# Optimization experiments

Measured on AMD Instinct MI355X. Metric: run time of the kernel, lower is better.

Reference implementation:

```python
import jax, jax.numpy as jnp
import numpy as np

N = 50000
E = 800000
EPS = 1e-16
NEG_SLOPE = 0.2

def setup_inputs() -> dict:
    key = jax.random.key(0)
    ks = jax.random.split(key, 10)
    s = lambda fan: 1.0 / np.sqrt(fan)
    return {
        "x": jax.random.normal(ks[0], (N, 128), dtype=jnp.float32),
        "edge_index": jax.random.randint(ks[1], (2, E), 0, N, dtype=jnp.int64),
        "W1": jax.random.normal(ks[2], (128, 4 * 32), dtype=jnp.float32) * s(128),
        "att_src1": jax.random.normal(ks[3], (4, 32), dtype=jnp.float32) * s(32),
        "att_dst1": jax.random.normal(ks[4], (4, 32), dtype=jnp.float32) * s(32),
        "b1": jnp.zeros((128,), dtype=jnp.float32),
        "W2": jax.random.normal(ks[5], (128, 2), dtype=jnp.float32) * s(128),
        "att_src2": jax.random.normal(ks[6], (1, 2), dtype=jnp.float32) * s(2),
        "att_dst2": jax.random.normal(ks[7], (1, 2), dtype=jnp.float32) * s(2),
        "b2": jnp.zeros((2,), dtype=jnp.float32),
    }

def _gat_conv(x, src, dst, W, att_src, att_dst, bias, heads, out_ch, concat):
    n = x.shape[0]
    h = (x @ W).reshape(n, heads, out_ch)                      # [N,H,C]
    a_src = jnp.sum(h * att_src[None], axis=-1)                # [N,H]
    a_dst = jnp.sum(h * att_dst[None], axis=-1)                # [N,H]
    e = jax.nn.leaky_relu(a_src[src] + a_dst[dst], NEG_SLOPE)  # [Etot,H]
    # segment softmax over incoming edges per destination node
    m = jax.ops.segment_max(e, dst, num_segments=n)            # [N,H]
    m = jnp.where(jnp.isfinite(m), m, 0.0)
    ex = jnp.exp(e - m[dst])
    denom = jax.ops.segment_sum(ex, dst, num_segments=n)       # [N,H]
    alpha = ex / (denom[dst] + EPS)                            # [Etot,H]
    out = jax.ops.segment_sum(alpha[:, :, None] * h[src], dst, num_segments=n)  # [N,H,C]
    if concat:
        out = out.reshape(n, heads * out_ch)
    else:
        out = out.mean(axis=1)
    return out + bias

def reference(x, edge_index, W1, att_src1, att_dst1, b1, W2, att_src2, att_dst2, b2):
    n = x.shape[0]
    # PyG GATConv adds self-loops by default
    loops = jnp.arange(n, dtype=edge_index.dtype)
    src = jnp.concatenate([edge_index[0], loops])
    dst = jnp.concatenate([edge_index[1], loops])
    # dropout is identity at inference
    h = jax.nn.elu(_gat_conv(x, src, dst, W1, att_src1, att_dst1, b1, 4, 32, True))
    h = _gat_conv(h, src, dst, W2, att_src2, att_dst2, b2, 1, 2, False)
    return jax.nn.log_softmax(h, axis=1)
```

## Files before the change

kernel.cpp:

```cpp
#include <hip/hip_runtime.h>
#include <hip/hip_bf16.h>

#define NN 50000
#define EE 800000
#define CAP 64
#define CSTRIDE 16
#define NEG_SLOPE 0.2f
#define EPSF 1e-16f
#define BUILD_BLOCKS 4096
#define GEMM_BLOCKS ((NN + 63) / 64)
#define NPAIRS (EE / 2)

typedef unsigned int uint32;
typedef __attribute__((ext_vector_type(8))) short short8;
typedef __attribute__((ext_vector_type(4))) float floatx4;

__device__ __forceinline__ unsigned short f2bf(float f) {
  unsigned int u = __float_as_uint(f);
  unsigned int r = (u + 0x7fffu + ((u >> 16) & 1u)) >> 16;
  return (unsigned short)r;
}
__device__ __forceinline__ float bf_lo(uint32 v) { return __uint_as_float(v << 16); }
__device__ __forceinline__ float bf_hi(uint32 v) { return __uint_as_float(v & 0xffff0000u); }
__device__ __forceinline__ float lrelu(float e) { return fmaxf(e, NEG_SLOPE * e); }

__global__ __launch_bounds__(256) void prep_zero_k(
    const float* __restrict__ W1, unsigned short* __restrict__ Wt,
    int* __restrict__ counts) {
  const int step = gridDim.x * 256;
  const int t0 = blockIdx.x * 256 + threadIdx.x;
  for (int i = t0; i < NN * CSTRIDE; i += step)
    counts[i] = ((i & (CSTRIDE - 1)) == 0) ? 1 : 0;
  for (int i = t0; i < 128 * 128; i += step) {
    int k = i >> 7, c = i & 127;
    Wt[c * 128 + k] = f2bf(W1[i]);
  }
}

__device__ __forceinline__ void do_build(int b, const int* __restrict__ ei,
                                         int* __restrict__ counts,
                                         int* __restrict__ csr) {
  const int range = b & 7;
  const int lo = range * (NN / 8);
  const int hi = lo + (NN / 8);
  const int group = b >> 3;
  const int tid0 = group * 256 + threadIdx.x;
  const int stride = (BUILD_BLOCKS >> 3) * 256;

  { int n = lo + tid0; if (n < hi) csr[n * CAP] = n; }

  const int2* __restrict__ dst2 = (const int2*)(ei + EE);
  const int2* __restrict__ src2 = (const int2*)(ei);
  for (int p = tid0; p < NPAIRS; p += stride) {
    int2 d2 = dst2[p];
    int2 s2 = src2[p];
    if (d2.x >= lo && d2.x < hi) {
      int r = atomicAdd(&counts[d2.x * CSTRIDE], 1);
      if (r < CAP) csr[d2.x * CAP + r] = s2.x;
    }
    if (d2.y >= lo && d2.y < hi) {
      int r = atomicAdd(&counts[d2.y * CSTRIDE], 1);
      if (r < CAP) csr[d2.y * CAP + r] = s2.y;
    }
  }
}

__device__ __forceinline__ void do_gemm_tile(
    int tile, const float* __restrict__ x, const unsigned short* __restrict__ Wt,
    const float* __restrict__ att_src1, const float* __restrict__ att_dst1,
    uint32* __restrict__ h1b, float* __restrict__ as1, float* __restrict__ ad1) {
  const int t    = threadIdx.x;
  const int wave = t >> 6;
  const int lane = t & 63;
  const int quad = lane >> 4;
  const int col  = lane & 15;
  const int nodeBase = tile * 64 + wave * 16;

  floatx4 acc[8];
  #pragma unroll
  for (int i = 0; i < 8; i++) acc[i] = (floatx4){0.f, 0.f, 0.f, 0.f};

  int mread = nodeBase + col; if (mread >= NN) mread = NN - 1;
  const float* __restrict__ xrow = x + (size_t)mread * 128 + quad * 8;
  const unsigned short* __restrict__ bbase = Wt + col * 128 + quad * 8;

  #pragma unroll
  for (int ks = 0; ks < 4; ks++) {
    float4 a0 = *(const float4*)(xrow + ks * 32);
    float4 a1 = *(const float4*)(xrow + ks * 32 + 4);
    union { short8 v; unsigned short u[8]; } af;
    af.u[0] = f2bf(a0.x); af.u[1] = f2bf(a0.y);
    af.u[2] = f2bf(a0.z); af.u[3] = f2bf(a0.w);
    af.u[4] = f2bf(a1.x); af.u[5] = f2bf(a1.y);
    af.u[6] = f2bf(a1.z); af.u[7] = f2bf(a1.w);
    #pragma unroll
    for (int tt = 0; tt < 8; tt++) {
      short8 bf = *(const short8*)(bbase + tt * 16 * 128 + ks * 32);
      acc[tt] = __builtin_amdgcn_mfma_f32_16x16x32_bf16(af.v, bf, acc[tt], 0, 0, 0);
    }
  }

  float asv[8], adv[8];
  #pragma unroll
  for (int tt = 0; tt < 8; tt++) {
    asv[tt] = att_src1[tt * 16 + col];
    adv[tt] = att_dst1[tt * 16 + col];
  }

  #pragma unroll
  for (int r = 0; r < 4; r++) {
    const int gn = nodeBase + quad * 4 + r;
    const bool live = (gn < NN);
    #pragma unroll
    for (int tt = 0; tt < 8; tt++) {
      float v = acc[tt][r];
      float w = __shfl_xor(v, 1, 64);
      if (live && ((col & 1) == 0)) {
        uint32 pk = (uint32)f2bf(v) | ((uint32)f2bf(w) << 16);
        h1b[(size_t)gn * 64 + tt * 8 + (col >> 1)] = pk;
      }
    }
    #pragma unroll
    for (int h = 0; h < 4; h++) {
      float ps = acc[2 * h][r] * asv[2 * h] + acc[2 * h + 1][r] * asv[2 * h + 1];
      float pd = acc[2 * h][r] * adv[2 * h] + acc[2 * h + 1][r] * adv[2 * h + 1];
      #pragma unroll
      for (int off = 1; off < 16; off <<= 1) {
        ps += __shfl_xor(ps, off, 64);
        pd += __shfl_xor(pd, off, 64);
      }
      if (live && col == 0) {
        as1[gn * 4 + h] = ps;
        ad1[gn * 4 + h] = pd;
      }
    }
  }
}

__global__ __launch_bounds__(256) void work_k(
    const int* __restrict__ ei, int* __restrict__ counts, int* __restrict__ csr,
    const float* __restrict__ x, const unsigned short* __restrict__ Wt,
    const float* __restrict__ att_src1, const float* __restrict__ att_dst1,
    uint32* __restrict__ h1b, float* __restrict__ as1, float* __restrict__ ad1) {
  const int b = blockIdx.x;
  if (b < BUILD_BLOCKS) {
    do_build(b, ei, counts, csr);
  } else {
    do_gemm_tile(b - BUILD_BLOCKS, x, Wt, att_src1, att_dst1, h1b, as1, ad1);
  }
}

__global__ __launch_bounds__(256) void agg1_k(
    const int* __restrict__ counts, const int* __restrict__ csr,
    const uint32* __restrict__ h1b, const float* __restrict__ as1,
    const float* __restrict__ ad1, const float* __restrict__ b1,
    const float* __restrict__ W2, const float* __restrict__ att_src2,
    const float* __restrict__ att_dst2, float4* __restrict__ rec) {
  const int lane = threadIdx.x & 63;
  const int wv = threadIdx.x >> 6;
  const int hd = lane >> 4;
  const int n = __builtin_amdgcn_readfirstlane(blockIdx.x * 4 + wv);

  int cnt = counts[n * CSTRIDE];
  cnt = __builtin_amdgcn_readfirstlane(cnt < CAP ? cnt : CAP);
  const int* __restrict__ row = csr + n * CAP;
  const float adv = ad1[n * 4 + hd];

  float den = 0.f, accx = 0.f, accy = 0.f;
  int j = 0;
  for (; j + 3 < cnt; j += 4) {
    int s0 = __builtin_amdgcn_readfirstlane(row[j]);
    int s1 = __builtin_amdgcn_readfirstlane(row[j + 1]);
    int s2 = __builtin_amdgcn_readfirstlane(row[j + 2]);
    int s3 = __builtin_amdgcn_readfirstlane(row[j + 3]);
    float e0 = as1[s0 * 4 + hd] + adv;
    float e1 = as1[s1 * 4 + hd] + adv;
    float e2 = as1[s2 * 4 + hd] + adv;
    float e3 = as1[s3 * 4 + hd] + adv;
    uint32 v0 = h1b[s0 * 64 + lane];
    uint32 v1 = h1b[s1 * 64 + lane];
    uint32 v2 = h1b[s2 * 64 + lane];
    uint32 v3 = h1b[s3 * 64 + lane];
    e0 = lrelu(e0); e1 = lrelu(e1); e2 = lrelu(e2); e3 = lrelu(e3);
    float x0 = __expf(e0), x1 = __expf(e1), x2 = __expf(e2), x3 = __expf(e3);
    den += (x0 + x1) + (x2 + x3);
    accx = fmaf(x0, bf_lo(v0), accx);
    accy = fmaf(x0, bf_hi(v0), accy);
    accx = fmaf(x1, bf_lo(v1), accx);
    accy = fmaf(x1, bf_hi(v1), accy);
    accx = fmaf(x2, bf_lo(v2), accx);
    accy = fmaf(x2, bf_hi(v2), accy);
    accx = fmaf(x3, bf_lo(v3), accx);
    accy = fmaf(x3, bf_hi(v3), accy);
  }
  for (; j < cnt; j++) {
    int s = __builtin_amdgcn_readfirstlane(row[j]);
    float e = lrelu(as1[s * 4 + hd] + adv);
    float ex = __expf(e);
    uint32 v = h1b[s * 64 + lane];
    den += ex;
    accx = fmaf(ex, bf_lo(v), accx);
    accy = fmaf(ex, bf_hi(v), accy);
  }

  float inv = 1.f / (den + EPSF);
  float2 bb = ((const float2*)b1)[lane];
  float ox = accx * inv + bb.x;
  float oy = accy * inv + bb.y;
  ox = (ox > 0.f) ? ox : (__expf(ox) - 1.f);
  oy = (oy > 0.f) ? oy : (__expf(oy) - 1.f);

  float4 wq = ((const float4*)W2)[lane];
  float p0 = ox * wq.x + oy * wq.z;
  float p1 = ox * wq.y + oy * wq.w;
  #pragma unroll
  for (int off = 32; off; off >>= 1) {
    p0 += __shfl_xor(p0, off, 64);
    p1 += __shfl_xor(p1, off, 64);
  }
  if (lane == 0) {
    rec[n] = make_float4(p0, p1,
                         p0 * att_src2[0] + p1 * att_src2[1],
                         p0 * att_dst2[0] + p1 * att_dst2[1]);
  }
}

__global__ __launch_bounds__(256) void agg2_k(
    const int* __restrict__ counts, const int* __restrict__ csr,
    const float4* __restrict__ rec, const float* __restrict__ b2,
    float* __restrict__ out) {
  int i = blockIdx.x * 256 + threadIdx.x;
  if (i >= NN * 8) return;
  int n = i >> 3;
  int sub = i & 7;
  const float adv = rec[n].w;
  int cnt = counts[n * CSTRIDE];
  cnt = cnt < CAP ? cnt : CAP;
  const int* __restrict__ row = csr + n * CAP;

  float den = 0.f, a0 = 0.f, a1 = 0.f;
  for (int j = sub; j < cnt; j += 8) {
    int s = row[j];
    float4 rs = rec[s];
    float e = lrelu(rs.z + adv);
    float ex = __expf(e);
    den += ex;
    a0 = fmaf(ex, rs.x, a0);
    a1 = fmaf(ex, rs.y, a1);
  }
  #pragma unroll
  for (int off = 4; off; off >>= 1) {
    den += __shfl_down(den, off, 8);
    a0  += __shfl_down(a0, off, 8);
    a1  += __shfl_down(a1, off, 8);
  }
  if (sub == 0) {
    float inv = 1.f / (den + EPSF);
    float o0 = a0 * inv + b2[0];
    float o1 = a1 * inv + b2[1];
    float mx = fmaxf(o0, o1);
    float lse = mx + __logf(__expf(o0 - mx) + __expf(o1 - mx));
    *(float2*)&out[n * 2] = make_float2(o0 - lse, o1 - lse);
  }
}

extern "C" void kernel_launch(void* const* d_in, const int* in_sizes, int n_in,
                              void* d_out, int out_size, void* d_ws, size_t ws_size,
                              hipStream_t stream) {
  const float* x        = (const float*)d_in[0];
  const int*   ei       = (const int*)d_in[1];
  const float* W1       = (const float*)d_in[2];
  const float* att_src1 = (const float*)d_in[3];
  const float* att_dst1 = (const float*)d_in[4];
  const float* b1       = (const float*)d_in[5];
  const float* W2       = (const float*)d_in[6];
  const float* att_src2 = (const float*)d_in[7];
  const float* att_dst2 = (const float*)d_in[8];
  const float* b2       = (const float*)d_in[9];
  float* out = (float*)d_out;

  char* p = (char*)d_ws;
  auto alloc = [&](size_t bytes) {
    char* r = p;
    p += (bytes + 255) & ~size_t(255);
    return r;
  };
  uint32* h1b  = (uint32*)alloc(sizeof(uint32) * NN * 64);
  float* as1   = (float*)alloc(sizeof(float) * NN * 4);
  float* ad1   = (float*)alloc(sizeof(float) * NN * 4);
  float4* rec  = (float4*)alloc(sizeof(float4) * NN);
  int*   counts = (int*)alloc(sizeof(int) * NN * CSTRIDE);
  int*   csr   = (int*)alloc(sizeof(int) * NN * CAP);
  unsigned short* Wt = (unsigned short*)alloc(sizeof(unsigned short) * 128 * 128);

  prep_zero_k<<<512, 256, 0, stream>>>(W1, Wt, counts);
  work_k<<<BUILD_BLOCKS + GEMM_BLOCKS, 256, 0, stream>>>(
      ei, counts, csr, x, Wt, att_src1, att_dst1, h1b, as1, ad1);
  agg1_k<<<NN / 4, 256, 0, stream>>>(counts, csr, h1b, as1, ad1, b1, W2,
                                     att_src2, att_dst2, rec);
  agg2_k<<<(NN * 8 + 255) / 256, 256, 0, stream>>>(counts, csr, rec, b2, out);
}
```

Before: 188.9 us.

## Fold W1 transpose into GEMM blocks via LDS and replace prep kernel with memset

Result: faster. 172.1 us (-8.9%).

```diff
diff --git a/kernel.cpp b/kernel.cpp
--- a/kernel.cpp
+++ b/kernel.cpp
@@ -10,6 +10,7 @@
 #define BUILD_BLOCKS 4096
 #define GEMM_BLOCKS ((NN + 63) / 64)
 #define NPAIRS (EE / 2)
+#define WROW 136
 
 typedef unsigned int uint32;
 typedef __attribute__((ext_vector_type(8))) short short8;
@@ -23,19 +24,6 @@
 __device__ __forceinline__ float bf_lo(uint32 v) { return __uint_as_float(v << 16); }
 __device__ __forceinline__ float bf_hi(uint32 v) { return __uint_as_float(v & 0xffff0000u); }
 __device__ __forceinline__ float lrelu(float e) { return fmaxf(e, NEG_SLOPE * e); }
-
-__global__ __launch_bounds__(256) void prep_zero_k(
-    const float* __restrict__ W1, unsigned short* __restrict__ Wt,
-    int* __restrict__ counts) {
-  const int step = gridDim.x * 256;
-  const int t0 = blockIdx.x * 256 + threadIdx.x;
-  for (int i = t0; i < NN * CSTRIDE; i += step)
-    counts[i] = ((i & (CSTRIDE - 1)) == 0) ? 1 : 0;
-  for (int i = t0; i < 128 * 128; i += step) {
-    int k = i >> 7, c = i & 127;
-    Wt[c * 128 + k] = f2bf(W1[i]);
-  }
-}
 
 __device__ __forceinline__ void do_build(int b, const int* __restrict__ ei,
                                          int* __restrict__ counts,
@@ -56,17 +44,17 @@
     int2 s2 = src2[p];
     if (d2.x >= lo && d2.x < hi) {
       int r = atomicAdd(&counts[d2.x * CSTRIDE], 1);
-      if (r < CAP) csr[d2.x * CAP + r] = s2.x;
+      if (r < CAP - 1) csr[d2.x * CAP + r + 1] = s2.x;
     }
     if (d2.y >= lo && d2.y < hi) {
       int r = atomicAdd(&counts[d2.y * CSTRIDE], 1);
-      if (r < CAP) csr[d2.y * CAP + r] = s2.y;
+      if (r < CAP - 1) csr[d2.y * CAP + r + 1] = s2.y;
     }
   }
 }
 
 __device__ __forceinline__ void do_gemm_tile(
-    int tile, const float* __restrict__ x, const unsigned short* __restrict__ Wt,
+    int tile, const float* __restrict__ x, const unsigned short* __restrict__ WtL,
     const float* __restrict__ att_src1, const float* __restrict__ att_dst1,
     uint32* __restrict__ h1b, float* __restrict__ as1, float* __restrict__ ad1) {
   const int t    = threadIdx.x;
@@ -82,7 +70,7 @@
 
   int mread = nodeBase + col; if (mread >= NN) mread = NN - 1;
   const float* __restrict__ xrow = x + (size_t)mread * 128 + quad * 8;
-  const unsigned short* __restrict__ bbase = Wt + col * 128 + quad * 8;
+  const unsigned short* __restrict__ bbase = WtL + col * WROW + quad * 8;
 
   #pragma unroll
   for (int ks = 0; ks < 4; ks++) {
@@ -95,7 +83,7 @@
     af.u[6] = f2bf(a1.z); af.u[7] = f2bf(a1.w);
     #pragma unroll
     for (int tt = 0; tt < 8; tt++) {
-      short8 bf = *(const short8*)(bbase + tt * 16 * 128 + ks * 32);
+      short8 bf = *(const short8*)(bbase + tt * 16 * WROW + ks * 32);
       acc[tt] = __builtin_amdgcn_mfma_f32_16x16x32_bf16(af.v, bf, acc[tt], 0, 0, 0);
     }
   }
@@ -139,14 +127,28 @@
 
 __global__ __launch_bounds__(256) void work_k(
     const int* __restrict__ ei, int* __restrict__ counts, int* __restrict__ csr,
-    const float* __restrict__ x, const unsigned short* __restrict__ Wt,
+    const float* __restrict__ x, const float* __restrict__ W1,
     const float* __restrict__ att_src1, const float* __restrict__ att_dst1,
     uint32* __restrict__ h1b, float* __restrict__ as1, float* __restrict__ ad1) {
+  __shared__ unsigned short WtL[128 * WROW];
   const int b = blockIdx.x;
-  if (b < BUILD_BLOCKS) {
-    do_build(b, ei, counts, csr);
+  if (b < GEMM_BLOCKS) {
+    const int c  = threadIdx.x & 127;
+    const int kh = (threadIdx.x >> 7) * 4;
+    #pragma unroll
+    for (int k0 = kh; k0 < 128; k0 += 8) {
+      unsigned short w0 = f2bf(W1[(k0 + 0) * 128 + c]);
+      unsigned short w1 = f2bf(W1[(k0 + 1) * 128 + c]);
+      unsigned short w2 = f2bf(W1[(k0 + 2) * 128 + c]);
+      unsigned short w3 = f2bf(W1[(k0 + 3) * 128 + c]);
+      uint32 lo = (uint32)w0 | ((uint32)w1 << 16);
+      uint32 hi = (uint32)w2 | ((uint32)w3 << 16);
+      *(uint2*)&WtL[c * WROW + k0] = make_uint2(lo, hi);
+    }
+    __syncthreads();
+    do_gemm_tile(b, x, WtL, att_src1, att_dst1, h1b, as1, ad1);
   } else {
-    do_gemm_tile(b - BUILD_BLOCKS, x, Wt, att_src1, att_dst1, h1b, as1, ad1);
+    do_build(b - GEMM_BLOCKS, ei, counts, csr);
   }
 }
 
@@ -161,7 +163,7 @@
   const int hd = lane >> 4;
   const int n = __builtin_amdgcn_readfirstlane(blockIdx.x * 4 + wv);
 
-  int cnt = counts[n * CSTRIDE];
+  int cnt = counts[n * CSTRIDE] + 1;
   cnt = __builtin_amdgcn_readfirstlane(cnt < CAP ? cnt : CAP);
   const int* __restrict__ row = csr + n * CAP;
   const float adv = ad1[n * 4 + hd];
@@ -234,7 +236,7 @@
   int n = i >> 3;
   int sub = i & 7;
   const float adv = rec[n].w;
-  int cnt = counts[n * CSTRIDE];
+  int cnt = counts[n * CSTRIDE] + 1;
   cnt = cnt < CAP ? cnt : CAP;
   const int* __restrict__ row = csr + n * CAP;
 
@@ -291,11 +293,10 @@
   float4* rec  = (float4*)alloc(sizeof(float4) * NN);
   int*   counts = (int*)alloc(sizeof(int) * NN * CSTRIDE);
   int*   csr   = (int*)alloc(sizeof(int) * NN * CAP);
-  unsigned short* Wt = (unsigned short*)alloc(sizeof(unsigned short) * 128 * 128);
-
-  prep_zero_k<<<512, 256, 0, stream>>>(W1, Wt, counts);
-  work_k<<<BUILD_BLOCKS + GEMM_BLOCKS, 256, 0, stream>>>(
-      ei, counts, csr, x, Wt, att_src1, att_dst1, h1b, as1, ad1);
+
+  hipMemsetAsync(counts, 0, sizeof(int) * NN * CSTRIDE, stream);
+  work_k<<<GEMM_BLOCKS + BUILD_BLOCKS, 256, 0, stream>>>(
+      ei, counts, csr, x, W1, att_src1, att_dst1, h1b, as1, ad1);
   agg1_k<<<NN / 4, 256, 0, stream>>>(counts, csr, h1b, as1, ad1, b1, W2,
                                      att_src2, att_dst2, rec);
   agg2_k<<<(NN * 8 + 255) / 256, 256, 0, stream>>>(counts, csr, rec, b2, out);
```
